# Kernel tuning notes

Hardware: AMD Instinct MI355X
Metric: run time of the kernel (lower is better)

## Reference

```python
import jax, jax.numpy as jnp
import numpy as np

# dims (match init_kwargs / input_specs)
K = 2      # sampling size k
B = 4      # batch
V = 2000   # vocab_size == number of graph nodes
D = 64     # embedding_dim
H = 4      # n_heads
DH = 64    # hidden units per head (n_hidden_units[0])
P = 128    # penultimate_hidden_unit
ALPHA = 0.2
NEG = -9e15  # large negative used by GAT to mask non-edges before softmax


def leaky_relu(v):
    return jnp.where(v >= 0, v, ALPHA * v)


def setup_inputs() -> dict:
    key = jax.random.key(0)
    ks = jax.random.split(key, 10)
    x = (jax.random.uniform(ks[0], (K, B, V)) < 0.1).astype(jnp.float32)
    E = jax.random.normal(ks[1], (V, D))                                 # embedding_weight (normal init)
    W = jax.random.normal(ks[2], (H, D, DH)) * (1.0 / np.sqrt(D))        # per-head GAT weight
    a1 = jax.random.normal(ks[3], (H, DH)) * 0.1                         # attention vec, src half
    a2 = jax.random.normal(ks[4], (H, DH)) * 0.1                         # attention vec, dst half
    cls_w = jax.random.normal(ks[5], (H * DH,))                          # cls_weight
    ac1 = jax.random.normal(ks[6], (H * DH,)) * 0.1                      # CLS attention vec halves
    ac2 = jax.random.normal(ks[7], (H * DH,)) * 0.1
    dense_W = jax.random.normal(ks[8], (H * DH, P)) * (1.0 / np.sqrt(H * DH))
    dense_b = jnp.zeros((P,), dtype=jnp.float32)
    return dict(x=x, E=E, W=W, a1=a1, a2=a2, cls_w=cls_w, ac1=ac1, ac2=ac2,
                dense_W=dense_W, dense_b=dense_b)


def gat_block(feat, mask, W, a1, a2):
    # feat: [B,V,Fin], mask: [B,V,V] bool (adj>0 support from outer product)
    Wh = jnp.einsum('bvf,hfo->bhvo', feat, W)                 # [B,H,V,DH]
    f1 = jnp.einsum('bhvo,ho->bhv', Wh, a1)
    f2 = jnp.einsum('bhvo,ho->bhv', Wh, a2)
    e = leaky_relu(f1[:, :, :, None] + f2[:, :, None, :])     # [B,H,V,V]
    e = jnp.where(mask[:, None, :, :], e, NEG)
    attn = jax.nn.softmax(e, axis=-1)
    out = jax.nn.elu(jnp.einsum('bhvu,bhuo->bhvo', attn, Wh))  # concat=True -> elu
    b, h, v, o = out.shape
    return out.transpose(0, 2, 1, 3).reshape(b, v, h * o)      # concat heads -> [B,V,H*DH]


def reference(x, E, W, a1, a2, cls_w, ac1, ac2, dense_W, dense_b):
    latents = [jnp.broadcast_to(cls_w, (B, cls_w.shape[0]))]   # CLS token per sample
    for i in range(K):
        xi = x[i]                                              # [B,V]
        present = xi > 0
        mask = present[:, :, None] & present[:, None, :]       # adj = outer(x,x) > 0
        feat = xi[:, :, None] * E[None]                        # mask embeddings by presence
        feat = gat_block(feat, mask, W, a1, a2)                # single hidden GAT layer
        latent = xi[:, :, None] * feat                         # [B,V,H*DH]
        latents.append(jnp.max(latent, axis=1))                # max-pool over nodes
    h = jnp.stack(latents, axis=1)                             # [B,K+1,F]
    cls = h[:, 0]
    e = leaky_relu((cls @ ac1)[:, None] + h @ ac2)             # [B,K+1]
    attn = jax.nn.softmax(e, axis=-1)
    pooled = jnp.einsum('bk,bkf->bf', attn, h)                 # CLS attention pooling
    return jax.nn.elu(pooled @ dense_W + dense_b)              # activation(dense(.))
```

## Files before the change

kernel.cpp:

```cpp
#include <hip/hip_runtime.h>
#include <hip/hip_bf16.h>

#define KK 2
#define BB 4
#define VV 2000
#define DD 64
#define HH 4
#define DHH 64
#define PP 128
#define ALPHA_ 0.2f

#define RPB 32
#define YB  8

typedef __attribute__((ext_vector_type(8))) short bf16x8;
typedef __attribute__((ext_vector_type(4))) float f32x4;

__device__ __forceinline__ float lrelu(float z) { return fmaxf(z, ALPHA_ * z); }
__device__ __forceinline__ float elu_(float z)  { return z > 0.f ? z : expm1f(z); }
__device__ __forceinline__ short f2bf(float f) {
  __hip_bfloat16 h = __float2bfloat16(f);
  return *reinterpret_cast<short*>(&h);
}
__device__ __forceinline__ float agent_acq_load(const float* p) {
  return __hip_atomic_load(p, __ATOMIC_ACQUIRE, __HIP_MEMORY_SCOPE_AGENT);
}

#define OFF_EW   0
#define OFF_F1   512000
#define OFF_F2   520000
#define OFF_LAT  528000
#define OFF_CNT  530048
#define OFF_S    530056
#define OFF_CTR  546056

__global__ __launch_bounds__(256) void k_pre(
    const float* __restrict__ E, const float* __restrict__ W,
    const float* __restrict__ a1, const float* __restrict__ a2,
    const float* __restrict__ x,
    float* __restrict__ EW, float* __restrict__ F1, float* __restrict__ F2,
    int* __restrict__ S, int* __restrict__ cnt, float* __restrict__ lat,
    int* __restrict__ ctr) {
  const int bid = blockIdx.x;
  const int wave = threadIdx.x >> 6, lane = threadIdx.x & 63;
  if (bid < 2000) {
    const int h = bid / 500;
    const int v = (bid % 500) * 4 + wave;
    bool pres = false;
#pragma unroll
    for (int kb = 0; kb < KK * BB; ++kb) pres |= (x[kb * VV + v] > 0.f);
    if (!pres) return;
    const float* Wh = W + h * DD * DHH;
    const float* Ev = E + v * DD;
    float acc = 0.f;
#pragma unroll 8
    for (int d = 0; d < DD; ++d) acc = fmaf(Ev[d], Wh[d * DHH + lane], acc);
    EW[(size_t)(h * VV + v) * DHH + lane] = acc;
    float r1 = acc * a1[h * DHH + lane];
    float r2 = acc * a2[h * DHH + lane];
#pragma unroll
    for (int s = 32; s; s >>= 1) { r1 += __shfl_xor(r1, s); r2 += __shfl_xor(r2, s); }
    if (lane == 0) { F1[h * VV + v] = r1; F2[h * VV + v] = r2; }
  } else {
    if (wave != 0) return;
    const int kb = bid - 2000;
    if (kb == 0)
      for (int i = lane; i < 36 * 16; i += 64) ctr[i] = 0;
    for (int i = lane; i < 256; i += 64) lat[kb * 256 + i] = 0.f;
    const float* xr = x + kb * VV;
    int base = 0;
    for (int t = 0; t * 64 < VV; ++t) {
      const int v = t * 64 + lane;
      const bool f = (v < VV) && (xr[v] > 0.f);
      const unsigned long long m = __ballot(f);
      if (f) S[kb * VV + base + __popcll(m & ((1ull << lane) - 1ull))] = v;
      base += __popcll(m);
    }
    if (lane == 0) cnt[kb] = base;
  }
}

__global__ __launch_bounds__(256) void k_attn(
    const float* __restrict__ EW, const float* __restrict__ F1,
    const float* __restrict__ F2, const int* __restrict__ S,
    const int* __restrict__ cnt, float* __restrict__ lat,
    const float* __restrict__ cls_w, const float* __restrict__ ac1,
    const float* __restrict__ ac2, const float* __restrict__ dW,
    const float* __restrict__ db, float* __restrict__ out,
    int* __restrict__ ctr) {
  __shared__ int   Sl[2048];
  __shared__ float G2l[2048];
  __shared__ float SF1[RPB], SM[RPB], SIV[RPB];
  __shared__ float pooled[256];
  __shared__ float fin[2][PP];
  __shared__ float red[4][4];
  __shared__ int s_fin;

  const int kb = blockIdx.x;
  const int h  = blockIdx.z;
  const int tid = threadIdx.x;
  const int wave = tid >> 6, lane = tid & 63;
  const int n = cnt[kb];
  const int nt = (n + RPB - 1) / RPB;

  if ((int)blockIdx.y < nt) {
    const int nup = (n + 31) & ~31;
    const int* Skb = S + kb * VV;
    const float* F2h = F2 + h * VV;
    const float* F1h = F1 + h * VV;
    const float* EWh = EW + (size_t)h * VV * DHH;

    for (int j = tid; j < nup; j += 256) {
      const int v = (j < n) ? Skb[j] : Skb[0];
      Sl[j] = v;
      G2l[j] = (j < n) ? F2h[v] : 0.f;
    }
    __syncthreads();

    const int col = (wave << 4) | (lane & 15);
    const int q   = lane >> 4;
    const float* EWcol = EWh + col;

    for (int tile = blockIdx.y; tile < nt; tile += YB) {
      const int r0w = tile * RPB + wave * 8;
      bool act[8]; float f1r[8];
#pragma unroll
      for (int i = 0; i < 8; ++i) {
        const int r = r0w + i;
        act[i] = r < n;
        f1r[i] = F1h[Sl[act[i] ? r : 0]];
      }
      float m[8];
#pragma unroll
      for (int i = 0; i < 8; ++i) m[i] = -3.4e38f;
      for (int jb = lane; jb < n; jb += 64) {
        const float g = G2l[jb];
#pragma unroll
        for (int i = 0; i < 8; ++i) m[i] = fmaxf(m[i], lrelu(f1r[i] + g));
      }
#pragma unroll
      for (int s = 32; s; s >>= 1)
#pragma unroll
        for (int i = 0; i < 8; ++i) m[i] = fmaxf(m[i], __shfl_xor(m[i], s));
      float sm[8];
#pragma unroll
      for (int i = 0; i < 8; ++i) sm[i] = 0.f;
      for (int jb = lane; jb < n; jb += 64) {
        const float g = G2l[jb];
#pragma unroll
        for (int i = 0; i < 8; ++i) sm[i] += __expf(lrelu(f1r[i] + g) - m[i]);
      }
#pragma unroll
      for (int s = 32; s; s >>= 1)
#pragma unroll
        for (int i = 0; i < 8; ++i) sm[i] += __shfl_xor(sm[i], s);

      __syncthreads();
      if (lane == 0) {
#pragma unroll
        for (int i = 0; i < 8; ++i) {
          SF1[wave * 8 + i] = f1r[i];
          SM[wave * 8 + i]  = m[i];
          SIV[wave * 8 + i] = act[i] ? (1.f / sm[i]) : 0.f;
        }
      }
      __syncthreads();

      const int rl = lane & 15;
      const float f1a = SF1[rl],      ma = SM[rl],      ia = SIV[rl];
      const float f1b = SF1[16 + rl], mb = SM[16 + rl], ib = SIV[16 + rl];
      f32x4 acc0 = {0.f, 0.f, 0.f, 0.f}, acc1 = {0.f, 0.f, 0.f, 0.f};
      for (int kc = 0; kc < nup; kc += 32) {
        const int kq = kc + q * 8;
        const int4 va = *reinterpret_cast<const int4*>(&Sl[kq]);
        const int4 vb = *reinterpret_cast<const int4*>(&Sl[kq + 4]);
        const float4 ga = *reinterpret_cast<const float4*>(&G2l[kq]);
        const float4 gb = *reinterpret_cast<const float4*>(&G2l[kq + 4]);
        float bv[8];
        bv[0] = EWcol[(size_t)va.x * DHH];
        bv[1] = EWcol[(size_t)va.y * DHH];
        bv[2] = EWcol[(size_t)va.z * DHH];
        bv[3] = EWcol[(size_t)va.w * DHH];
        bv[4] = EWcol[(size_t)vb.x * DHH];
        bv[5] = EWcol[(size_t)vb.y * DHH];
        bv[6] = EWcol[(size_t)vb.z * DHH];
        bv[7] = EWcol[(size_t)vb.w * DHH];
        const float g[8] = {ga.x, ga.y, ga.z, ga.w, gb.x, gb.y, gb.z, gb.w};
        float pa[8], pb[8];
#pragma unroll
        for (int t = 0; t < 8; ++t) {
          const float gt = g[t];
          pa[t] = __expf(lrelu(f1a + gt) - ma) * ia;
          pb[t] = __expf(lrelu(f1b + gt) - mb) * ib;
        }
        if (kc + 32 > n) {
#pragma unroll
          for (int t = 0; t < 8; ++t)
            if (kq + t >= n) { pa[t] = 0.f; pb[t] = 0.f; }
        }
        bf16x8 A0, A1, Bf;
#pragma unroll
        for (int t = 0; t < 8; ++t) {
          A0[t] = f2bf(pa[t]);
          A1[t] = f2bf(pb[t]);
          Bf[t] = f2bf(bv[t]);
        }
        acc0 = __builtin_amdgcn_mfma_f32_16x16x32_bf16(A0, Bf, acc0, 0, 0, 0);
        acc1 = __builtin_amdgcn_mfma_f32_16x16x32_bf16(A1, Bf, acc1, 0, 0, 0);
      }
      float vmax = -3.4e38f;
#pragma unroll
      for (int r = 0; r < 4; ++r) {
        const int row0 = tile * RPB + (q << 2) + r;
        const int row1 = row0 + 16;
        if (row0 < n) vmax = fmaxf(vmax, acc0[r]);
        if (row1 < n) vmax = fmaxf(vmax, acc1[r]);
      }
      if (vmax > 0.f) {
        const int old = atomicMax(
            reinterpret_cast<int*>(&lat[kb * 256 + h * DHH + col]),
            __float_as_int(vmax));
        asm volatile("" : : "v"(old));
      }
    }
  }

  __syncthreads();
  if (tid == 0) {
    int fin_ = 0;
    const int l = atomicAdd(&ctr[(kb * HH + h) * 16], 1);
    if (l == YB - 1) {
      const int r = atomicAdd(&ctr[(32 + (kb & 3)) * 16], 1);
      fin_ = (r == KK * HH - 1);
    }
    s_fin = fin_;
  }
  __syncthreads();
  if (!s_fin) return;

  const int b = kb & 3;
  const float cw = cls_w[tid];
  const float l0 = agent_acq_load(&lat[(0 * BB + b) * 256 + tid]);
  const float l1 = agent_acq_load(&lat[(1 * BB + b) * 256 + tid]);
  float t0 = cw * ac1[tid];
  float t1 = cw * ac2[tid];
  float t2 = l0 * ac2[tid];
  float t3 = l1 * ac2[tid];
#pragma unroll
  for (int s = 32; s; s >>= 1) {
    t0 += __shfl_xor(t0, s); t1 += __shfl_xor(t1, s);
    t2 += __shfl_xor(t2, s); t3 += __shfl_xor(t3, s);
  }
  if (lane == 0) { red[wave][0] = t0; red[wave][1] = t1; red[wave][2] = t2; red[wave][3] = t3; }
  __syncthreads();
  const float ca1 = red[0][0] + red[1][0] + red[2][0] + red[3][0];
  const float d0  = red[0][1] + red[1][1] + red[2][1] + red[3][1];
  const float d1  = red[0][2] + red[1][2] + red[2][2] + red[3][2];
  const float d2  = red[0][3] + red[1][3] + red[2][3] + red[3][3];
  const float e0 = lrelu(ca1 + d0), e1 = lrelu(ca1 + d1), e2 = lrelu(ca1 + d2);
  const float mm = fmaxf(e0, fmaxf(e1, e2));
  const float x0 = __expf(e0 - mm), x1 = __expf(e1 - mm), x2 = __expf(e2 - mm);
  const float invs = 1.f / (x0 + x1 + x2);
  pooled[tid] = (x0 * cw + x1 * l0 + x2 * l1) * invs;
  __syncthreads();
  {
    const int o = tid & (PP - 1), half = tid >> 7;
    const float* dWc = dW + (half * 128) * PP + o;
    const float* pl = &pooled[half * 128];
    float a0 = 0.f, a1v = 0.f, a2v = 0.f, a3v = 0.f;
    float a4 = 0.f, a5 = 0.f, a6 = 0.f, a7 = 0.f;
#pragma unroll
    for (int f = 0; f < 128; f += 8) {
      a0  = fmaf(pl[f + 0], dWc[(f + 0) * PP], a0);
      a1v = fmaf(pl[f + 1], dWc[(f + 1) * PP], a1v);
      a2v = fmaf(pl[f + 2], dWc[(f + 2) * PP], a2v);
      a3v = fmaf(pl[f + 3], dWc[(f + 3) * PP], a3v);
      a4  = fmaf(pl[f + 4], dWc[(f + 4) * PP], a4);
      a5  = fmaf(pl[f + 5], dWc[(f + 5) * PP], a5);
      a6  = fmaf(pl[f + 6], dWc[(f + 6) * PP], a6);
      a7  = fmaf(pl[f + 7], dWc[(f + 7) * PP], a7);
    }
    fin[half][o] = ((a0 + a1v) + (a2v + a3v)) + ((a4 + a5) + (a6 + a7));
  }
  __syncthreads();
  if (tid < PP) out[b * PP + tid] = elu_(db[tid] + fin[0][tid] + fin[1][tid]);
}

extern "C" void kernel_launch(void* const* d_in, const int* in_sizes, int n_in,
                              void* d_out, int out_size, void* d_ws, size_t ws_size,
                              hipStream_t stream) {
  const float* x     = (const float*)d_in[0];
  const float* E     = (const float*)d_in[1];
  const float* W     = (const float*)d_in[2];
  const float* a1    = (const float*)d_in[3];
  const float* a2    = (const float*)d_in[4];
  const float* cls_w = (const float*)d_in[5];
  const float* ac1   = (const float*)d_in[6];
  const float* ac2   = (const float*)d_in[7];
  const float* dW    = (const float*)d_in[8];
  const float* db    = (const float*)d_in[9];
  float* out = (float*)d_out;

  float* ws  = (float*)d_ws;
  float* EW  = ws + OFF_EW;
  float* F1  = ws + OFF_F1;
  float* F2  = ws + OFF_F2;
  float* LAT = ws + OFF_LAT;
  int*   CNT = (int*)(ws + OFF_CNT);
  int*   S   = (int*)(ws + OFF_S);
  int*   CTR = (int*)(ws + OFF_CTR);

  k_pre<<<2008, 256, 0, stream>>>(E, W, a1, a2, x, EW, F1, F2, S, CNT, LAT, CTR);
  k_attn<<<dim3(KK * BB, YB, HH), 256, 0, stream>>>(EW, F1, F2, S, CNT, LAT,
                                                    cls_w, ac1, ac2, dW, db, out, CTR);
}
```

Before: 33.71 us.

## Fuse projection into attention kernel with per-block bf16 node features in LDS

Drops the separate pre-pass kernel. Each attention block now compacts its present-node list, computes the E·W projection and both attention logits for its head straight into shared memory as bf16, and feeds MFMA from LDS instead of gathering from global memory. Workspace zeroing moves to a memset. The cost is redundant projection work across the y-blocks, and a hard cap of 384 present nodes per sample, which holds for about 10% density but would silently truncate denser inputs.

Result: slower. 70.89 us (+110.3%).

```diff
diff --git a/kernel.cpp b/kernel.cpp
--- a/kernel.cpp
+++ b/kernel.cpp
@@ -12,6 +12,9 @@
 
 #define RPB 32
 #define YB  8
+#define NWV 4
+#define N_CAP 384
+#define LSTR 66
 
 typedef __attribute__((ext_vector_type(8))) short bf16x8;
 typedef __attribute__((ext_vector_type(4))) float f32x4;
@@ -26,109 +29,93 @@
   return __hip_atomic_load(p, __ATOMIC_ACQUIRE, __HIP_MEMORY_SCOPE_AGENT);
 }
 
-#define OFF_EW   0
-#define OFF_F1   512000
-#define OFF_F2   520000
-#define OFF_LAT  528000
-#define OFF_CNT  530048
-#define OFF_S    530056
-#define OFF_CTR  546056
-
-__global__ __launch_bounds__(256) void k_pre(
+#define OFF_LAT 0
+#define OFF_CTR 2048
+
+__global__ __launch_bounds__(256, 1) void k_fused(
     const float* __restrict__ E, const float* __restrict__ W,
     const float* __restrict__ a1, const float* __restrict__ a2,
-    const float* __restrict__ x,
-    float* __restrict__ EW, float* __restrict__ F1, float* __restrict__ F2,
-    int* __restrict__ S, int* __restrict__ cnt, float* __restrict__ lat,
-    int* __restrict__ ctr) {
-  const int bid = blockIdx.x;
-  const int wave = threadIdx.x >> 6, lane = threadIdx.x & 63;
-  if (bid < 2000) {
-    const int h = bid / 500;
-    const int v = (bid % 500) * 4 + wave;
-    bool pres = false;
-#pragma unroll
-    for (int kb = 0; kb < KK * BB; ++kb) pres |= (x[kb * VV + v] > 0.f);
-    if (!pres) return;
-    const float* Wh = W + h * DD * DHH;
-    const float* Ev = E + v * DD;
-    float acc = 0.f;
-#pragma unroll 8
-    for (int d = 0; d < DD; ++d) acc = fmaf(Ev[d], Wh[d * DHH + lane], acc);
-    EW[(size_t)(h * VV + v) * DHH + lane] = acc;
-    float r1 = acc * a1[h * DHH + lane];
-    float r2 = acc * a2[h * DHH + lane];
-#pragma unroll
-    for (int s = 32; s; s >>= 1) { r1 += __shfl_xor(r1, s); r2 += __shfl_xor(r2, s); }
-    if (lane == 0) { F1[h * VV + v] = r1; F2[h * VV + v] = r2; }
-  } else {
-    if (wave != 0) return;
-    const int kb = bid - 2000;
-    if (kb == 0)
-      for (int i = lane; i < 36 * 16; i += 64) ctr[i] = 0;
-    for (int i = lane; i < 256; i += 64) lat[kb * 256 + i] = 0.f;
+    const float* __restrict__ x, const float* __restrict__ cls_w,
+    const float* __restrict__ ac1, const float* __restrict__ ac2,
+    const float* __restrict__ dW, const float* __restrict__ db,
+    float* __restrict__ out, float* __restrict__ lat, int* __restrict__ ctr) {
+  __shared__ unsigned short EWb[N_CAP][LSTR];
+  __shared__ int   Sl[N_CAP];
+  __shared__ float G1l[N_CAP], G2l[N_CAP];
+  __shared__ float SF1[RPB], SM[RPB], SIV[RPB];
+  __shared__ float pooled[256], finp[2][PP], red[4][4];
+  __shared__ int s_n, s_fin;
+
+  const int kb = blockIdx.x;
+  const int y  = blockIdx.y;
+  const int h  = blockIdx.z;
+  const int tid = threadIdx.x;
+  const int wave = tid >> 6, lane = tid & 63;
+
+  if (wave == 0) {
     const float* xr = x + kb * VV;
     int base = 0;
     for (int t = 0; t * 64 < VV; ++t) {
       const int v = t * 64 + lane;
       const bool f = (v < VV) && (xr[v] > 0.f);
-      const unsigned long long m = __ballot(f);
-      if (f) S[kb * VV + base + __popcll(m & ((1ull << lane) - 1ull))] = v;
-      base += __popcll(m);
-    }
-    if (lane == 0) cnt[kb] = base;
-  }
-}
-
-__global__ __launch_bounds__(256) void k_attn(
-    const float* __restrict__ EW, const float* __restrict__ F1,
-    const float* __restrict__ F2, const int* __restrict__ S,
-    const int* __restrict__ cnt, float* __restrict__ lat,
-    const float* __restrict__ cls_w, const float* __restrict__ ac1,
-    const float* __restrict__ ac2, const float* __restrict__ dW,
-    const float* __restrict__ db, float* __restrict__ out,
-    int* __restrict__ ctr) {
-  __shared__ int   Sl[2048];
-  __shared__ float G2l[2048];
-  __shared__ float SF1[RPB], SM[RPB], SIV[RPB];
-  __shared__ float pooled[256];
-  __shared__ float fin[2][PP];
-  __shared__ float red[4][4];
-  __shared__ int s_fin;
-
-  const int kb = blockIdx.x;
-  const int h  = blockIdx.z;
-  const int tid = threadIdx.x;
-  const int wave = tid >> 6, lane = tid & 63;
-  const int n = cnt[kb];
+      const unsigned long long mm = __ballot(f);
+      if (f) {
+        const int pos = base + __popcll(mm & ((1ull << lane) - 1ull));
+        if (pos < N_CAP) Sl[pos] = v;
+      }
+      base += __popcll(mm);
+    }
+    if (lane == 0) s_n = (base < N_CAP) ? base : N_CAP;
+  }
+  __syncthreads();
+  const int n = s_n;
+  const int nup = (n + 31) & ~31;
+
+  {
+    const float a1v = a1[h * DHH + lane];
+    const float a2v = a2[h * DHH + lane];
+    float wcol[DD];
+#pragma unroll
+    for (int d = 0; d < DD; ++d) wcol[d] = W[(h * DD + d) * DHH + lane];
+#pragma unroll 2
+    for (int r = wave; r < nup; r += NWV) {
+      if (r < n) {
+        const int vu = __builtin_amdgcn_readfirstlane(Sl[r]);
+        const float* Ev = E + vu * DD;
+        float c0 = 0.f, c1 = 0.f, c2 = 0.f, c3 = 0.f;
+#pragma unroll
+        for (int d = 0; d < DD; d += 4) {
+          c0 = fmaf(Ev[d + 0], wcol[d + 0], c0);
+          c1 = fmaf(Ev[d + 1], wcol[d + 1], c1);
+          c2 = fmaf(Ev[d + 2], wcol[d + 2], c2);
+          c3 = fmaf(Ev[d + 3], wcol[d + 3], c3);
+        }
+        const float acc = (c0 + c1) + (c2 + c3);
+        EWb[r][lane] = (unsigned short)f2bf(acc);
+        float r1 = acc * a1v, r2 = acc * a2v;
+#pragma unroll
+        for (int s = 32; s; s >>= 1) { r1 += __shfl_xor(r1, s); r2 += __shfl_xor(r2, s); }
+        if (lane == 0) { G1l[r] = r1; G2l[r] = r2; }
+      } else {
+        EWb[r][lane] = 0;
+        if (lane == 0) { G1l[r] = 0.f; G2l[r] = 0.f; }
+      }
+    }
+  }
+  __syncthreads();
+
   const int nt = (n + RPB - 1) / RPB;
-
-  if ((int)blockIdx.y < nt) {
-    const int nup = (n + 31) & ~31;
-    const int* Skb = S + kb * VV;
-    const float* F2h = F2 + h * VV;
-    const float* F1h = F1 + h * VV;
-    const float* EWh = EW + (size_t)h * VV * DHH;
-
-    for (int j = tid; j < nup; j += 256) {
-      const int v = (j < n) ? Skb[j] : Skb[0];
-      Sl[j] = v;
-      G2l[j] = (j < n) ? F2h[v] : 0.f;
-    }
-    __syncthreads();
-
+  if (y < nt) {
     const int col = (wave << 4) | (lane & 15);
     const int q   = lane >> 4;
-    const float* EWcol = EWh + col;
-
-    for (int tile = blockIdx.y; tile < nt; tile += YB) {
+    for (int tile = y; tile < nt; tile += YB) {
       const int r0w = tile * RPB + wave * 8;
       bool act[8]; float f1r[8];
 #pragma unroll
       for (int i = 0; i < 8; ++i) {
         const int r = r0w + i;
         act[i] = r < n;
-        f1r[i] = F1h[Sl[act[i] ? r : 0]];
+        f1r[i] = G1l[act[i] ? r : 0];
       }
       float m[8];
 #pragma unroll
@@ -172,20 +159,12 @@
       f32x4 acc0 = {0.f, 0.f, 0.f, 0.f}, acc1 = {0.f, 0.f, 0.f, 0.f};
       for (int kc = 0; kc < nup; kc += 32) {
         const int kq = kc + q * 8;
-        const int4 va = *reinterpret_cast<const int4*>(&Sl[kq]);
-        const int4 vb = *reinterpret_cast<const int4*>(&Sl[kq + 4]);
         const float4 ga = *reinterpret_cast<const float4*>(&G2l[kq]);
         const float4 gb = *reinterpret_cast<const float4*>(&G2l[kq + 4]);
-        float bv[8];
-        bv[0] = EWcol[(size_t)va.x * DHH];
-        bv[1] = EWcol[(size_t)va.y * DHH];
-        bv[2] = EWcol[(size_t)va.z * DHH];
-        bv[3] = EWcol[(size_t)va.w * DHH];
-        bv[4] = EWcol[(size_t)vb.x * DHH];
-        bv[5] = EWcol[(size_t)vb.y * DHH];
-        bv[6] = EWcol[(size_t)vb.z * DHH];
-        bv[7] = EWcol[(size_t)vb.w * DHH];
         const float g[8] = {ga.x, ga.y, ga.z, ga.w, gb.x, gb.y, gb.z, gb.w};
+        bf16x8 Bf;
+#pragma unroll
+        for (int t = 0; t < 8; ++t) Bf[t] = (short)EWb[kq + t][col];
         float pa[8], pb[8];
 #pragma unroll
         for (int t = 0; t < 8; ++t) {
@@ -198,13 +177,9 @@
           for (int t = 0; t < 8; ++t)
             if (kq + t >= n) { pa[t] = 0.f; pb[t] = 0.f; }
         }
-        bf16x8 A0, A1, Bf;
-#pragma unroll
-        for (int t = 0; t < 8; ++t) {
-          A0[t] = f2bf(pa[t]);
-          A1[t] = f2bf(pb[t]);
-          Bf[t] = f2bf(bv[t]);
-        }
+        bf16x8 A0, A1;
+#pragma unroll
+        for (int t = 0; t < 8; ++t) { A0[t] = f2bf(pa[t]); A1[t] = f2bf(pb[t]); }
         acc0 = __builtin_amdgcn_mfma_f32_16x16x32_bf16(A0, Bf, acc0, 0, 0, 0);
         acc1 = __builtin_amdgcn_mfma_f32_16x16x32_bf16(A1, Bf, acc1, 0, 0, 0);
       }
@@ -240,8 +215,8 @@
 
   const int b = kb & 3;
   const float cw = cls_w[tid];
-  const float l0 = agent_acq_load(&lat[(0 * BB + b) * 256 + tid]);
-  const float l1 = agent_acq_load(&lat[(1 * BB + b) * 256 + tid]);
+  const float l0 = fmaxf(agent_acq_load(&lat[(0 * BB + b) * 256 + tid]), 0.f);
+  const float l1 = fmaxf(agent_acq_load(&lat[(1 * BB + b) * 256 + tid]), 0.f);
   float t0 = cw * ac1[tid];
   float t1 = cw * ac2[tid];
   float t2 = l0 * ac2[tid];
@@ -267,23 +242,23 @@
     const int o = tid & (PP - 1), half = tid >> 7;
     const float* dWc = dW + (half * 128) * PP + o;
     const float* pl = &pooled[half * 128];
-    float a0 = 0.f, a1v = 0.f, a2v = 0.f, a3v = 0.f;
+    float a0 = 0.f, b1 = 0.f, b2 = 0.f, b3 = 0.f;
     float a4 = 0.f, a5 = 0.f, a6 = 0.f, a7 = 0.f;
 #pragma unroll
     for (int f = 0; f < 128; f += 8) {
-      a0  = fmaf(pl[f + 0], dWc[(f + 0) * PP], a0);
-      a1v = fmaf(pl[f + 1], dWc[(f + 1) * PP], a1v);
-      a2v = fmaf(pl[f + 2], dWc[(f + 2) * PP], a2v);
-      a3v = fmaf(pl[f + 3], dWc[(f + 3) * PP], a3v);
-      a4  = fmaf(pl[f + 4], dWc[(f + 4) * PP], a4);
-      a5  = fmaf(pl[f + 5], dWc[(f + 5) * PP], a5);
-      a6  = fmaf(pl[f + 6], dWc[(f + 6) * PP], a6);
-      a7  = fmaf(pl[f + 7], dWc[(f + 7) * PP], a7);
-    }
-    fin[half][o] = ((a0 + a1v) + (a2v + a3v)) + ((a4 + a5) + (a6 + a7));
-  }
-  __syncthreads();
-  if (tid < PP) out[b * PP + tid] = elu_(db[tid] + fin[0][tid] + fin[1][tid]);
+      a0 = fmaf(pl[f + 0], dWc[(f + 0) * PP], a0);
+      b1 = fmaf(pl[f + 1], dWc[(f + 1) * PP], b1);
+      b2 = fmaf(pl[f + 2], dWc[(f + 2) * PP], b2);
+      b3 = fmaf(pl[f + 3], dWc[(f + 3) * PP], b3);
+      a4 = fmaf(pl[f + 4], dWc[(f + 4) * PP], a4);
+      a5 = fmaf(pl[f + 5], dWc[(f + 5) * PP], a5);
+      a6 = fmaf(pl[f + 6], dWc[(f + 6) * PP], a6);
+      a7 = fmaf(pl[f + 7], dWc[(f + 7) * PP], a7);
+    }
+    finp[half][o] = ((a0 + b1) + (b2 + b3)) + ((a4 + a5) + (a6 + a7));
+  }
+  __syncthreads();
+  if (tid < PP) out[b * PP + tid] = elu_(db[tid] + finp[0][tid] + finp[1][tid]);
 }
 
 extern "C" void kernel_launch(void* const* d_in, const int* in_sizes, int n_in,
@@ -302,15 +277,10 @@
   float* out = (float*)d_out;
 
   float* ws  = (float*)d_ws;
-  float* EW  = ws + OFF_EW;
-  float* F1  = ws + OFF_F1;
-  float* F2  = ws + OFF_F2;
   float* LAT = ws + OFF_LAT;
-  int*   CNT = (int*)(ws + OFF_CNT);
-  int*   S   = (int*)(ws + OFF_S);
   int*   CTR = (int*)(ws + OFF_CTR);
 
-  k_pre<<<2008, 256, 0, stream>>>(E, W, a1, a2, x, EW, F1, F2, S, CNT, LAT, CTR);
-  k_attn<<<dim3(KK * BB, YB, HH), 256, 0, stream>>>(EW, F1, F2, S, CNT, LAT,
-                                                    cls_w, ac1, ac2, dW, db, out, CTR);
-}
+  hipMemsetAsync(LAT, 0, (2048 + 576) * sizeof(float), stream);
+  k_fused<<<dim3(KK * BB, YB, HH), 256, 0, stream>>>(
+      E, W, a1, a2, x, cls_w, ac1, ac2, dW, db, out, LAT, CTR);
+}
```

## Move final dense epilogue into dedicated spin-waiting blocks with preloaded weights

Applied to the files above, without the earlier changes.

Instead of the last-arriving attention block doing the CLS pooling and dense layer, four dedicated blocks (one per batch) launch first. They preload their column of dense_W into registers, then spin on the per-batch completion counter before running the epilogue. This takes the dense-weight loads off the critical tail of the kernel. In exchange it adds spinning blocks that occupy CUs and a register-heavy path, and it relies on those blocks being scheduled early enough that they cannot deadlock.

Result: faster. 32.73 us (-2.9%).

```diff
diff --git a/kernel.cpp b/kernel.cpp
--- a/kernel.cpp
+++ b/kernel.cpp
@@ -12,6 +12,7 @@
 
 #define RPB 32
 #define YB  8
+#define NFIN 4
 
 typedef __attribute__((ext_vector_type(8))) short bf16x8;
 typedef __attribute__((ext_vector_type(4))) float f32x4;
@@ -23,6 +24,9 @@
   return *reinterpret_cast<short*>(&h);
 }
 __device__ __forceinline__ float agent_acq_load(const float* p) {
+  return __hip_atomic_load(p, __ATOMIC_ACQUIRE, __HIP_MEMORY_SCOPE_AGENT);
+}
+__device__ __forceinline__ int agent_acq_load_i(const int* p) {
   return __hip_atomic_load(p, __ATOMIC_ACQUIRE, __HIP_MEMORY_SCOPE_AGENT);
 }
 
@@ -92,18 +96,84 @@
   __shared__ float G2l[2048];
   __shared__ float SF1[RPB], SM[RPB], SIV[RPB];
   __shared__ float pooled[256];
-  __shared__ float fin[2][PP];
+  __shared__ float finp[2][PP];
   __shared__ float red[4][4];
-  __shared__ int s_fin;
-
-  const int kb = blockIdx.x;
-  const int h  = blockIdx.z;
+
+  const int bid = blockIdx.x;
   const int tid = threadIdx.x;
   const int wave = tid >> 6, lane = tid & 63;
+
+  if (bid < NFIN) {
+    const int b = bid;
+    const int o = tid & (PP - 1), half = tid >> 7;
+    float dwr[128];
+    const float* dWc = dW + (half * 128) * PP + o;
+#pragma unroll
+    for (int f = 0; f < 128; ++f) dwr[f] = dWc[f * PP];
+    const float cw = cls_w[tid];
+    const float v1 = ac1[tid], v2 = ac2[tid];
+    const float dbv = (tid < PP) ? db[tid] : 0.f;
+    {
+      float chk = 0.f;
+#pragma unroll
+      for (int f = 0; f < 128; ++f) chk += dwr[f];
+      asm volatile("" : : "v"(chk), "v"(cw), "v"(v1), "v"(v2), "v"(dbv));
+    }
+    if (tid == 0) {
+      while (agent_acq_load_i(&ctr[(32 + b) * 16]) < KK * HH)
+        __builtin_amdgcn_s_sleep(8);
+    }
+    __syncthreads();
+    const float l0 = agent_acq_load(&lat[(0 * BB + b) * 256 + tid]);
+    const float l1 = agent_acq_load(&lat[(1 * BB + b) * 256 + tid]);
+    float t0 = cw * v1, t1 = cw * v2, t2 = l0 * v2, t3 = l1 * v2;
+#pragma unroll
+    for (int s = 32; s; s >>= 1) {
+      t0 += __shfl_xor(t0, s); t1 += __shfl_xor(t1, s);
+      t2 += __shfl_xor(t2, s); t3 += __shfl_xor(t3, s);
+    }
+    if (lane == 0) { red[wave][0] = t0; red[wave][1] = t1; red[wave][2] = t2; red[wave][3] = t3; }
+    __syncthreads();
+    const float ca1 = red[0][0] + red[1][0] + red[2][0] + red[3][0];
+    const float d0  = red[0][1] + red[1][1] + red[2][1] + red[3][1];
+    const float d1  = red[0][2] + red[1][2] + red[2][2] + red[3][2];
+    const float d2  = red[0][3] + red[1][3] + red[2][3] + red[3][3];
+    const float e0 = lrelu(ca1 + d0), e1 = lrelu(ca1 + d1), e2 = lrelu(ca1 + d2);
+    const float mm = fmaxf(e0, fmaxf(e1, e2));
+    const float x0 = __expf(e0 - mm), x1 = __expf(e1 - mm), x2 = __expf(e2 - mm);
+    const float invs = 1.f / (x0 + x1 + x2);
+    pooled[tid] = (x0 * cw + x1 * l0 + x2 * l1) * invs;
+    __syncthreads();
+    {
+      const float* pl = &pooled[half * 128];
+      float a0 = 0.f, b1 = 0.f, b2 = 0.f, b3 = 0.f;
+      float a4 = 0.f, a5 = 0.f, a6 = 0.f, a7 = 0.f;
+#pragma unroll
+      for (int f = 0; f < 128; f += 8) {
+        a0 = fmaf(pl[f + 0], dwr[f + 0], a0);
+        b1 = fmaf(pl[f + 1], dwr[f + 1], b1);
+        b2 = fmaf(pl[f + 2], dwr[f + 2], b2);
+        b3 = fmaf(pl[f + 3], dwr[f + 3], b3);
+        a4 = fmaf(pl[f + 4], dwr[f + 4], a4);
+        a5 = fmaf(pl[f + 5], dwr[f + 5], a5);
+        a6 = fmaf(pl[f + 6], dwr[f + 6], a6);
+        a7 = fmaf(pl[f + 7], dwr[f + 7], a7);
+      }
+      finp[half][o] = ((a0 + b1) + (b2 + b3)) + ((a4 + a5) + (a6 + a7));
+    }
+    __syncthreads();
+    if (tid < PP) out[b * PP + tid] = elu_(dbv + finp[0][tid] + finp[1][tid]);
+    return;
+  }
+
+  const int idx = bid - NFIN;
+  const int kb = idx & 7;
+  const int y  = (idx >> 3) & 7;
+  const int h  = idx >> 6;
   const int n = cnt[kb];
   const int nt = (n + RPB - 1) / RPB;
 
-  if ((int)blockIdx.y < nt) {
+  if (y < nt) {
     const int nup = (n + 31) & ~31;
     const int* Skb = S + kb * VV;
     const float* F2h = F2 + h * VV;
@@ -121,7 +191,7 @@
     const int q   = lane >> 4;
     const float* EWcol = EWh + col;
 
-    for (int tile = blockIdx.y; tile < nt; tile += YB) {
+    for (int tile = y; tile < nt; tile += YB) {
       const int r0w = tile * RPB + wave * 8;
       bool act[8]; float f1r[8];
 #pragma unroll
@@ -227,63 +297,12 @@
 
   __syncthreads();
   if (tid == 0) {
-    int fin_ = 0;
     const int l = atomicAdd(&ctr[(kb * HH + h) * 16], 1);
     if (l == YB - 1) {
       const int r = atomicAdd(&ctr[(32 + (kb & 3)) * 16], 1);
-      fin_ = (r == KK * HH - 1);
-    }
-    s_fin = fin_;
+      asm volatile("" : : "v"(r));
+    }
   }
-  __syncthreads();
-  if (!s_fin) return;
-
-  const int b = kb & 3;
-  const float cw = cls_w[tid];
-  const float l0 = agent_acq_load(&lat[(0 * BB + b) * 256 + tid]);
-  const float l1 = agent_acq_load(&lat[(1 * BB + b) * 256 + tid]);
-  float t0 = cw * ac1[tid];
-  float t1 = cw * ac2[tid];
-  float t2 = l0 * ac2[tid];
-  float t3 = l1 * ac2[tid];
-#pragma unroll
-  for (int s = 32; s; s >>= 1) {
-    t0 += __shfl_xor(t0, s); t1 += __shfl_xor(t1, s);
-    t2 += __shfl_xor(t2, s); t3 += __shfl_xor(t3, s);
-  }
-  if (lane == 0) { red[wave][0] = t0; red[wave][1] = t1; red[wave][2] = t2; red[wave][3] = t3; }
-  __syncthreads();
-  const float ca1 = red[0][0] + red[1][0] + red[2][0] + red[3][0];
-  const float d0  = red[0][1] + red[1][1] + red[2][1] + red[3][1];
-  const float d1  = red[0][2] + red[1][2] + red[2][2] + red[3][2];
-  const float d2  = red[0][3] + red[1][3] + red[2][3] + red[3][3];
-  const float e0 = lrelu(ca1 + d0), e1 = lrelu(ca1 + d1), e2 = lrelu(ca1 + d2);
-  const float mm = fmaxf(e0, fmaxf(e1, e2));
-  const float x0 = __expf(e0 - mm), x1 = __expf(e1 - mm), x2 = __expf(e2 - mm);
-  const float invs = 1.f / (x0 + x1 + x2);
-  pooled[tid] = (x0 * cw + x1 * l0 + x2 * l1) * invs;
-  __syncthreads();
-  {
-    const int o = tid & (PP - 1), half = tid >> 7;
-    const float* dWc = dW + (half * 128) * PP + o;
-    const float* pl = &pooled[half * 128];
-    float a0 = 0.f, a1v = 0.f, a2v = 0.f, a3v = 0.f;
-    float a4 = 0.f, a5 = 0.f, a6 = 0.f, a7 = 0.f;
-#pragma unroll
-    for (int f = 0; f < 128; f += 8) {
-      a0  = fmaf(pl[f + 0], dWc[(f + 0) * PP], a0);
-      a1v = fmaf(pl[f + 1], dWc[(f + 1) * PP], a1v);
-      a2v = fmaf(pl[f + 2], dWc[(f + 2) * PP], a2v);
-      a3v = fmaf(pl[f + 3], dWc[(f + 3) * PP], a3v);
-      a4  = fmaf(pl[f + 4], dWc[(f + 4) * PP], a4);
-      a5  = fmaf(pl[f + 5], dWc[(f + 5) * PP], a5);
-      a6  = fmaf(pl[f + 6], dWc[(f + 6) * PP], a6);
-      a7  = fmaf(pl[f + 7], dWc[(f + 7) * PP], a7);
-    }
-    fin[half][o] = ((a0 + a1v) + (a2v + a3v)) + ((a4 + a5) + (a6 + a7));
-  }
-  __syncthreads();
-  if (tid < PP) out[b * PP + tid] = elu_(db[tid] + fin[0][tid] + fin[1][tid]);
 }
 
 extern "C" void kernel_launch(void* const* d_in, const int* in_sizes, int n_in,
@@ -311,6 +330,6 @@
   int*   CTR = (int*)(ws + OFF_CTR);
 
   k_pre<<<2008, 256, 0, stream>>>(E, W, a1, a2, x, EW, F1, F2, S, CNT, LAT, CTR);
-  k_attn<<<dim3(KK * BB, YB, HH), 256, 0, stream>>>(EW, F1, F2, S, CNT, LAT,
-                                                    cls_w, ac1, ac2, dW, db, out, CTR);
-}
+  k_attn<<<NFIN + KK * BB * YB * HH, 256, 0, stream>>>(
+      EW, F1, F2, S, CNT, LAT, cls_w, ac1, ac2, dW, db, out, CTR);
+}
```
